# Optimization experiments

Measured on AMD Instinct MI355X. Metric: run time of the kernel, lower is better.

The kernel has to match this reference:

```python
import jax, jax.numpy as jnp
import numpy as np

N_NODES = 100000
N_EDGES = 3200000
D_FEAT = 128


def setup_inputs() -> dict:
    key = jax.random.key(0)
    k1, k2, k3, k4 = jax.random.split(key, 4)
    row = jax.random.randint(k1, (N_EDGES,), 0, N_NODES, dtype=jnp.int32)
    col = jax.random.randint(k2, (N_EDGES,), 0, N_NODES, dtype=jnp.int32)
    vals = jax.random.uniform(k3, (N_EDGES,), dtype=jnp.float32)
    embeds = jax.random.normal(k4, (N_NODES, D_FEAT), dtype=jnp.float32)
    return {"row": row, "col": col, "vals": vals, "embeds": embeds}


def reference(row, col, vals, embeds):
    # torch.spmm(adj, embeds) with adj in COO form (row, col, vals):
    # out[i, :] = sum_{e : row[e]==i} vals[e] * embeds[col[e], :]
    msgs = embeds[col] * vals[:, None]          # [E, d] gather + scale
    out = jax.ops.segment_sum(msgs, row, num_segments=embeds.shape[0])  # [N, d]
    return out
```

## Files before the change

kernel.cpp:

```cpp
#include <hip/hip_runtime.h>
#include <hip/hip_fp16.h>

#define D_FEAT 128

constexpr int SCAN_BLOCK = 256;
constexpr int SCAN_ITEMS = 8;
constexpr int SCAN_CHUNK = SCAN_BLOCK * SCAN_ITEMS;

constexpr int BUCKET_SHIFT = 7;
constexpr int TILE_ROWS = 1 << BUCKET_SHIFT;
constexpr int NB_MAX = 1024;
constexpr int PART_TILE = 4096;
constexpr int CAP = 6144;

__global__ void __launch_bounds__(256) spmm_atomic_kernel(
    const int* __restrict__ row, const int* __restrict__ col,
    const float* __restrict__ vals, const float* __restrict__ embeds,
    float* __restrict__ out, int n_edges)
{
    const int lane = threadIdx.x & 63;
    const int wave_in_block = threadIdx.x >> 6;
    const int waves_per_block = blockDim.x >> 6;
    const int n_waves = gridDim.x * waves_per_block;
    for (int e = blockIdx.x * waves_per_block + wave_in_block; e < n_edges; e += n_waves) {
        const int r = row[e];
        const int c = col[e];
        const float v = vals[e];
        const float2 emb = *reinterpret_cast<const float2*>(&embeds[(size_t)c * D_FEAT + lane * 2]);
        float* o = &out[(size_t)r * D_FEAT + lane * 2];
        atomicAdd(o, emb.x * v);
        atomicAdd(o + 1, emb.y * v);
    }
}


__global__ void __launch_bounds__(256) bucket_hist_kernel(
    const int* __restrict__ row, int* __restrict__ bucket_counts, int n_edges, int nb)
{
    __shared__ int cnt[NB_MAX];
    for (int b = threadIdx.x; b < nb; b += 256) cnt[b] = 0;
    __syncthreads();
    const int i = blockIdx.x * blockDim.x + threadIdx.x;
    const int stride = gridDim.x * blockDim.x;
    const int n4 = n_edges >> 2;
    for (int k = i; k < n4; k += stride) {
        int4 r4 = reinterpret_cast<const int4*>(row)[k];
        atomicAdd(&cnt[r4.x >> BUCKET_SHIFT], 1);
        atomicAdd(&cnt[r4.y >> BUCKET_SHIFT], 1);
        atomicAdd(&cnt[r4.z >> BUCKET_SHIFT], 1);
        atomicAdd(&cnt[r4.w >> BUCKET_SHIFT], 1);
    }
    for (int k = (n4 << 2) + i; k < n_edges; k += stride)
        atomicAdd(&cnt[row[k] >> BUCKET_SHIFT], 1);
    __syncthreads();
    for (int b = threadIdx.x; b < nb; b += 256) {
        int c = cnt[b];
        if (c) atomicAdd(&bucket_counts[b], c);
    }
}

__global__ void __launch_bounds__(1024) bucket_scan_kernel(
    const int* __restrict__ bucket_counts, int* __restrict__ bucket_ptr,
    int* __restrict__ bucket_fill, int nb)
{
    __shared__ int lds[1024];
    const int t = threadIdx.x;
    lds[t] = (t < nb) ? bucket_counts[t] : 0;
    __syncthreads();
    for (int off = 1; off < 1024; off <<= 1) {
        int x = (t >= off) ? lds[t - off] : 0;
        __syncthreads();
        lds[t] += x;
        __syncthreads();
    }
    const int excl = (t == 0) ? 0 : lds[t - 1];
    if (t <= nb) bucket_ptr[t] = excl;
    if (t < nb)  bucket_fill[t] = excl;
}

__global__ void __launch_bounds__(256) bucket_init_padded_kernel(
    int* __restrict__ bucket_ptr, int* __restrict__ bucket_fill, int nb, int cap_b)
{
    int b = blockIdx.x * blockDim.x + threadIdx.x;
    if (b < nb) {
        bucket_ptr[b]  = b * cap_b;
        bucket_fill[b] = b * cap_b;
    }
}

__global__ void __launch_bounds__(256) partition_kernel(
    const int* __restrict__ row, const int* __restrict__ col, const float* __restrict__ vals,
    int* __restrict__ bucket_fill, uint2* __restrict__ tmp, int n_edges, int nb)
{
    __shared__ int cnt[NB_MAX];
    __shared__ int start[NB_MAX];
    const int tid = threadIdx.x;
    const int base = blockIdx.x * PART_TILE;

    for (int b = tid; b < NB_MAX; b += 256) cnt[b] = 0;
    __syncthreads();

    #pragma unroll
    for (int k = 0; k < PART_TILE / 1024; ++k) {
        int idx = (base >> 2) + k * 256 + tid;
        if (idx * 4 + 3 < n_edges) {
            int4 r4 = reinterpret_cast<const int4*>(row)[idx];
            atomicAdd(&cnt[r4.x >> BUCKET_SHIFT], 1);
            atomicAdd(&cnt[r4.y >> BUCKET_SHIFT], 1);
            atomicAdd(&cnt[r4.z >> BUCKET_SHIFT], 1);
            atomicAdd(&cnt[r4.w >> BUCKET_SHIFT], 1);
        } else {
            for (int j = 0; j < 4; ++j) {
                int e = idx * 4 + j;
                if (e < n_edges) atomicAdd(&cnt[row[e] >> BUCKET_SHIFT], 1);
            }
        }
    }
    __syncthreads();

    for (int b = tid; b < nb; b += 256) {
        int c = cnt[b];
        if (c > 0) start[b] = atomicAdd(&bucket_fill[b], c);
    }
    __syncthreads();

    #pragma unroll
    for (int k = 0; k < PART_TILE / 1024; ++k) {
        int idx = (base >> 2) + k * 256 + tid;
        if (idx * 4 + 3 < n_edges) {
            int4  r4 = reinterpret_cast<const int4*>(row)[idx];
            int4  c4 = reinterpret_cast<const int4*>(col)[idx];
            float4 v4 = reinterpret_cast<const float4*>(vals)[idx];
            const int rs[4]   = {r4.x, r4.y, r4.z, r4.w};
            const int cs[4]   = {c4.x, c4.y, c4.z, c4.w};
            const float vs[4] = {v4.x, v4.y, v4.z, v4.w};
            #pragma unroll
            for (int j = 0; j < 4; ++j) {
                int r = rs[j];
                int b = r >> BUCKET_SHIFT;
                int slot = atomicSub(&cnt[b], 1) - 1;
                unsigned hb = (unsigned)__half_as_ushort(__float2half(vs[j]));
                uint2 p;
                p.x = ((unsigned)(r & (TILE_ROWS - 1)) << 17) | (unsigned)cs[j];
                p.y = hb | (hb << 16);
                tmp[start[b] + slot] = p;
            }
        } else {
            for (int j = 0; j < 4; ++j) {
                int e = idx * 4 + j;
                if (e < n_edges) {
                    int r = row[e];
                    int b = r >> BUCKET_SHIFT;
                    int slot = atomicSub(&cnt[b], 1) - 1;
                    unsigned hb = (unsigned)__half_as_ushort(__float2half(vals[e]));
                    uint2 p;
                    p.x = ((unsigned)(r & (TILE_ROWS - 1)) << 17) | (unsigned)col[e];
                    p.y = hb | (hb << 16);
                    tmp[start[b] + slot] = p;
                }
            }
        }
    }
}

__global__ void __launch_bounds__(256) convert_kernel(
    const float* __restrict__ embeds, unsigned short* __restrict__ out16, int n4)
{
    int i = blockIdx.x * blockDim.x + threadIdx.x;
    int stride = gridDim.x * blockDim.x;
    for (; i < n4; i += stride) {
        float4 f = *reinterpret_cast<const float4*>(&embeds[(size_t)i * 4]);
        ushort4 o;
        o.x = __half_as_ushort(__float2half(f.x));
        o.y = __half_as_ushort(__float2half(f.y));
        o.z = __half_as_ushort(__float2half(f.z));
        o.w = __half_as_ushort(__float2half(f.w));
        *reinterpret_cast<ushort4*>(&out16[(size_t)i * 4]) = o;
    }
}

__device__ __forceinline__ __half2 u2h2(unsigned u)
{
    return *reinterpret_cast<__half2*>(&u);
}

__global__ void __launch_bounds__(1024, 8) spmm_bucket_sorted_kernel(
    const uint2* __restrict__ tmp, const int* __restrict__ bucket_ptr,
    const int* __restrict__ bucket_fill,
    const unsigned short* __restrict__ embeds16, float* __restrict__ out, int n_nodes)
{
    __shared__ uint2 sedge[CAP];
    __shared__ int cnt[TILE_ROWS];
    __shared__ int rstart[TILE_ROWS];
    __shared__ int rcur[TILE_ROWS];
    __shared__ int sscan[TILE_ROWS];

    const int b = blockIdx.x;
    const int lo = bucket_ptr[b];
    const int hi = bucket_fill[b];
    const int t = threadIdx.x;
    const int lane = t & 63;
    const int h = lane >> 5;
    const int lq = lane & 31;
    const int w = t >> 6;

    __half2 acc[16];
    #pragma unroll
    for (int i = 0; i < 16; ++i) acc[i] = __float2half2_rn(0.f);

    for (int cur = lo; cur < hi; cur += CAP) {
        const int bcount = min(CAP, hi - cur);

        uint2 e[6];
        #pragma unroll
        for (int k = 0; k < 6; ++k) {
            int idx = t + k * 1024;
            if (idx < bcount) e[k] = tmp[cur + idx];
        }
        if (t < TILE_ROWS) { cnt[t] = 0; rcur[t] = 0; }
        __syncthreads();

        #pragma unroll
        for (int k = 0; k < 6; ++k) {
            int idx = t + k * 1024;
            if (idx < bcount) atomicAdd(&cnt[(e[k].x >> 17) & (TILE_ROWS - 1)], 1);
        }
        __syncthreads();

        if (t < TILE_ROWS) sscan[t] = cnt[t];
        __syncthreads();
        for (int off = 1; off < TILE_ROWS; off <<= 1) {
            int v = 0;
            if (t < TILE_ROWS && t >= off) v = sscan[t - off];
            __syncthreads();
            if (t < TILE_ROWS) sscan[t] += v;
            __syncthreads();
        }
        if (t < TILE_ROWS) rstart[t] = sscan[t] - cnt[t];
        __syncthreads();

        #pragma unroll
        for (int k = 0; k < 6; ++k) {
            int idx = t + k * 1024;
            if (idx < bcount) {
                int rl = (e[k].x >> 17) & (TILE_ROWS - 1);
                int pos = rstart[rl] + atomicAdd(&rcur[rl], 1);
                sedge[pos] = uint2{e[k].x & 0x1FFFFu, e[k].y};
            }
        }
        __syncthreads();

        #pragma unroll
        for (int rr = 0; rr < 8; ++rr) {
            const int r = w * 8 + rr;
            const int js = rstart[r];
            const int je = js + cnt[r];
            int j = js;
            for (; j + 7 < je; j += 8) {
                uint2 q0 = sedge[j + 0 + h];
                uint2 q1 = sedge[j + 2 + h];
                uint2 q2 = sedge[j + 4 + h];
                uint2 q3 = sedge[j + 6 + h];
                uint2 u0 = *reinterpret_cast<const uint2*>(&embeds16[((size_t)q0.x << 7) + lq * 4]);
                uint2 u1 = *reinterpret_cast<const uint2*>(&embeds16[((size_t)q1.x << 7) + lq * 4]);
                uint2 u2 = *reinterpret_cast<const uint2*>(&embeds16[((size_t)q2.x << 7) + lq * 4]);
                uint2 u3 = *reinterpret_cast<const uint2*>(&embeds16[((size_t)q3.x << 7) + lq * 4]);
                acc[2*rr]   = __hfma2(u2h2(q0.y), u2h2(u0.x), acc[2*rr]);
                acc[2*rr+1] = __hfma2(u2h2(q0.y), u2h2(u0.y), acc[2*rr+1]);
                acc[2*rr]   = __hfma2(u2h2(q1.y), u2h2(u1.x), acc[2*rr]);
                acc[2*rr+1] = __hfma2(u2h2(q1.y), u2h2(u1.y), acc[2*rr+1]);
                acc[2*rr]   = __hfma2(u2h2(q2.y), u2h2(u2.x), acc[2*rr]);
                acc[2*rr+1] = __hfma2(u2h2(q2.y), u2h2(u2.y), acc[2*rr+1]);
                acc[2*rr]   = __hfma2(u2h2(q3.y), u2h2(u3.x), acc[2*rr]);
                acc[2*rr+1] = __hfma2(u2h2(q3.y), u2h2(u3.y), acc[2*rr+1]);
            }
            for (; j + 1 < je; j += 2) {
                uint2 q = sedge[j + h];
                uint2 u = *reinterpret_cast<const uint2*>(&embeds16[((size_t)q.x << 7) + lq * 4]);
                acc[2*rr]   = __hfma2(u2h2(q.y), u2h2(u.x), acc[2*rr]);
                acc[2*rr+1] = __hfma2(u2h2(q.y), u2h2(u.y), acc[2*rr+1]);
            }
            if (j < je && h == 0) {
                uint2 q = sedge[j];
                uint2 u = *reinterpret_cast<const uint2*>(&embeds16[((size_t)q.x << 7) + lq * 4]);
                acc[2*rr]   = __hfma2(u2h2(q.y), u2h2(u.x), acc[2*rr]);
                acc[2*rr+1] = __hfma2(u2h2(q.y), u2h2(u.y), acc[2*rr+1]);
            }
        }
        __syncthreads();
    }

    float4 facc[8];
    #pragma unroll
    for (int rr = 0; rr < 8; ++rr) {
        float2 a = __half22float2(acc[2*rr]);
        float2 bq = __half22float2(acc[2*rr+1]);
        facc[rr] = float4{a.x, a.y, bq.x, bq.y};
        facc[rr].x += __shfl_xor(facc[rr].x, 32);
        facc[rr].y += __shfl_xor(facc[rr].y, 32);
        facc[rr].z += __shfl_xor(facc[rr].z, 32);
        facc[rr].w += __shfl_xor(facc[rr].w, 32);
    }

    const int rbase = b << BUCKET_SHIFT;
    #pragma unroll
    for (int k = 0; k < 4; ++k) {
        float4 a0 = facc[k];
        float4 a1 = facc[k + 4];
        float4 vv;
        vv.x = h ? a1.x : a0.x;
        vv.y = h ? a1.y : a0.y;
        vv.z = h ? a1.z : a0.z;
        vv.w = h ? a1.w : a0.w;
        int r = rbase + w * 8 + k + 4 * h;
        if (r < n_nodes)
            *reinterpret_cast<float4*>(&out[(size_t)r * D_FEAT + lq * 4]) = vv;
    }
}

__global__ void hist_kernel(const int* __restrict__ row, int* __restrict__ counts, int n)
{
    int i = blockIdx.x * blockDim.x + threadIdx.x;
    int stride = gridDim.x * blockDim.x;
    for (; i < n; i += stride) atomicAdd(&counts[row[i]], 1);
}

__global__ void __launch_bounds__(SCAN_BLOCK) scan1_kernel(
    const int* __restrict__ counts, int* __restrict__ scan_out,
    int* __restrict__ chunk_sums, int n)
{
    __shared__ int lds[SCAN_BLOCK];
    const int chunk = blockIdx.x;
    const int base = chunk * SCAN_CHUNK;
    const int tbase = base + threadIdx.x * SCAN_ITEMS;

    int pref[SCAN_ITEMS];
    int tsum = 0;
    for (int k = 0; k < SCAN_ITEMS; ++k) {
        int idx = tbase + k;
        int v = (idx < n) ? counts[idx] : 0;
        pref[k] = tsum;
        tsum += v;
    }
    lds[threadIdx.x] = tsum;
    __syncthreads();
    for (int off = 1; off < SCAN_BLOCK; off <<= 1) {
        int v = (threadIdx.x >= off) ? lds[threadIdx.x - off] : 0;
        __syncthreads();
        lds[threadIdx.x] += v;
        __syncthreads();
    }
    const int texcl = (threadIdx.x == 0) ? 0 : lds[threadIdx.x - 1];
    for (int k = 0; k < SCAN_ITEMS; ++k) {
        int idx = tbase + k;
        if (idx < n) scan_out[idx] = texcl + pref[k];
    }
    if (threadIdx.x == SCAN_BLOCK - 1) chunk_sums[chunk] = lds[SCAN_BLOCK - 1];
}

__global__ void scan2_kernel(int* chunk_sums, int nchunks)
{
    if (blockIdx.x == 0 && threadIdx.x == 0) {
        int acc = 0;
        for (int i = 0; i < nchunks; ++i) { int v = chunk_sums[i]; chunk_sums[i] = acc; acc += v; }
    }
}

__global__ void scan3_kernel(int* __restrict__ row_ptr, const int* __restrict__ chunk_sums,
                             int n, int n_edges)
{
    int i = blockIdx.x * blockDim.x + threadIdx.x;
    if (i < n) row_ptr[i] += chunk_sums[i / SCAN_CHUNK];
    if (i == 0) row_ptr[n] = n_edges;
}

__global__ void scatter_kernel(const int* __restrict__ row, const int* __restrict__ col,
                               const float* __restrict__ vals,
                               const int* __restrict__ row_ptr, int* __restrict__ row_fill,
                               uint2* __restrict__ sorted_cv, int n_edges)
{
    int i = blockIdx.x * blockDim.x + threadIdx.x;
    int stride = gridDim.x * blockDim.x;
    for (; i < n_edges; i += stride) {
        int r = row[i];
        int pos = row_ptr[r] + atomicAdd(&row_fill[r], 1);
        uint2 cv;
        cv.x = (unsigned)col[i];
        cv.y = __float_as_uint(vals[i]);
        sorted_cv[pos] = cv;
    }
}

__global__ void __launch_bounds__(256) spmm_csr_kernel(
    const int* __restrict__ row_ptr, const uint2* __restrict__ sorted_cv,
    const float* __restrict__ embeds, float* __restrict__ out, int n_rows)
{
    const int lane = threadIdx.x & 63;
    const int wid = (blockIdx.x * blockDim.x + threadIdx.x) >> 6;
    const int n_waves = (gridDim.x * blockDim.x) >> 6;

    for (int r = wid; r < n_rows; r += n_waves) {
        const int start = row_ptr[r];
        const int end   = row_ptr[r + 1];
        float2 acc = {0.f, 0.f};
        for (int j = start; j < end; ++j) {
            uint2 cv = sorted_cv[j];
            const float2 e = *reinterpret_cast<const float2*>(&embeds[(size_t)cv.x * D_FEAT + lane * 2]);
            const float v = __uint_as_float(cv.y);
            acc.x += v * e.x;
            acc.y += v * e.y;
        }
        *reinterpret_cast<float2*>(&out[(size_t)r * D_FEAT + lane * 2]) = acc;
    }
}

extern "C" void kernel_launch(void* const* d_in, const int* in_sizes, int n_in,
                              void* d_out, int out_size, void* d_ws, size_t ws_size,
                              hipStream_t stream) {
    const int*   row    = (const int*)d_in[0];
    const int*   col    = (const int*)d_in[1];
    const float* vals   = (const float*)d_in[2];
    const float* embeds = (const float*)d_in[3];
    float*       out    = (float*)d_out;

    const int n_edges = in_sizes[0];
    const int n_nodes = in_sizes[3] / D_FEAT;
    const int nchunks = (n_nodes + SCAN_CHUNK - 1) / SCAN_CHUNK;
    const int nb = (n_nodes + TILE_ROWS - 1) >> BUCKET_SHIFT;

    const int avg = n_edges / (nb > 0 ? nb : 1);
    const int cap_b = avg + avg / 4 + 256;

    char* base = (char*)d_ws;

    size_t offP = 0;
    uint2* tmpP           = (uint2*)(base + offP);             offP += ((size_t)nb * cap_b * 8 + 255) & ~(size_t)255;
    unsigned short* emb16P = (unsigned short*)(base + offP);   offP += ((size_t)n_nodes * D_FEAT * 2 + 255) & ~(size_t)255;
    int* bptrP            = (int*)(base + offP);               offP += (size_t)(nb + 1) * 4;
    int* bfillP           = (int*)(base + offP);               offP += (size_t)(nb + 1) * 4;

    size_t offS = 0;
    uint2* tmpS           = (uint2*)(base + offS);             offS += ((size_t)n_edges * 8 + 255) & ~(size_t)255;
    unsigned short* emb16S = (unsigned short*)(base + offS);   offS += ((size_t)n_nodes * D_FEAT * 2 + 255) & ~(size_t)255;
    int* bcntS            = (int*)(base + offS);               offS += (size_t)(nb + 1) * 4;
    int* bptrS            = (int*)(base + offS);               offS += (size_t)(nb + 1) * 4;
    int* bfillS           = (int*)(base + offS);               offS += (size_t)(nb + 1) * 4;

    const bool common_ok = (nb <= 1023) && (n_nodes < (1 << 17));
    const bool padded_ok  = common_ok && (offP <= ws_size);
    const bool scanned_ok = common_ok && (offS <= ws_size);

    if (!padded_ok && !scanned_ok) {
        size_t off2 = 0;
        uint2* s_cv = (uint2*)(base + off2); off2 += (size_t)n_edges * 8;
        int* rc  = (int*)(base + off2); off2 += (size_t)n_nodes * 4;
        int* rf  = (int*)(base + off2); off2 += (size_t)n_nodes * 4;
        int* rp  = (int*)(base + off2); off2 += (size_t)(n_nodes + 1) * 4;
        int* cs  = (int*)(base + off2); off2 += (size_t)nchunks * 4;
        if (off2 > ws_size) {
            hipMemsetAsync(d_out, 0, (size_t)out_size * sizeof(float), stream);
            spmm_atomic_kernel<<<2048, 256, 0, stream>>>(row, col, vals, embeds, out, n_edges);
            return;
        }
        hipMemsetAsync(rc, 0, (size_t)n_nodes * 2 * sizeof(int), stream);
        hist_kernel<<<2048, 256, 0, stream>>>(row, rc, n_edges);
        scan1_kernel<<<nchunks, SCAN_BLOCK, 0, stream>>>(rc, rp, cs, n_nodes);
        scan2_kernel<<<1, 64, 0, stream>>>(cs, nchunks);
        scan3_kernel<<<(n_nodes + 256) / 256, 256, 0, stream>>>(rp, cs, n_nodes, n_edges);
        scatter_kernel<<<2048, 256, 0, stream>>>(row, col, vals, rp, rf, s_cv, n_edges);
        spmm_csr_kernel<<<4096, 256, 0, stream>>>(rp, s_cv, embeds, out, n_nodes);
        return;
    }

    uint2* tmp;
    unsigned short* embeds16;
    int *bptr, *bfill;

    const int part_blocks = (n_edges + PART_TILE - 1) / PART_TILE;

    if (padded_ok) {
        tmp = tmpP; embeds16 = emb16P; bptr = bptrP; bfill = bfillP;
        bucket_init_padded_kernel<<<(nb + 255) / 256, 256, 0, stream>>>(bptr, bfill, nb, cap_b);
    } else {
        tmp = tmpS; embeds16 = emb16S; bptr = bptrS; bfill = bfillS;
        hipMemsetAsync(bcntS, 0, (size_t)(nb + 1) * sizeof(int), stream);
        bucket_hist_kernel<<<512, 256, 0, stream>>>(row, bcntS, n_edges, nb);
        bucket_scan_kernel<<<1, 1024, 0, stream>>>(bcntS, bptr, bfill, nb);
    }

    partition_kernel<<<part_blocks, 256, 0, stream>>>(row, col, vals, bfill, tmp, n_edges, nb);

    const int n4 = n_nodes * D_FEAT / 4;
    convert_kernel<<<4096, 256, 0, stream>>>(embeds, embeds16, n4);

    spmm_bucket_sorted_kernel<<<nb, 1024, 0, stream>>>(tmp, bptr, bfill, embeds16, out, n_nodes);
}
```

Before: 232.9 us.

## Halve bucket size and use persistent work-queue SpMM blocks with 16-lane row groups

Buckets now cover 64 rows instead of 128, which doubles the bucket count and halves the per-chunk edge capacity. The final SpMM kernel becomes persistent: 1024 blocks of 512 threads pull buckets from a global atomic counter. Each quarter-wave of 16 lanes handles a whole edge with 16-byte embedding loads, and partial sums are reduced across quarter-waves with shuffles. The aim is better load balance, wider per-lane loads, and cheaper in-block row sorting via a wave-level shuffle scan. In exchange it adds per-bucket barriers, a second pass over edges from global memory rather than registers, and extra shuffle reductions.

```diff
diff --git a/kernel.cpp b/kernel.cpp
--- a/kernel.cpp
+++ b/kernel.cpp
@@ -7,11 +7,11 @@
 constexpr int SCAN_ITEMS = 8;
 constexpr int SCAN_CHUNK = SCAN_BLOCK * SCAN_ITEMS;
 
-constexpr int BUCKET_SHIFT = 7;
+constexpr int BUCKET_SHIFT = 6;
 constexpr int TILE_ROWS = 1 << BUCKET_SHIFT;
-constexpr int NB_MAX = 1024;
+constexpr int NB_MAX = 2048;
 constexpr int PART_TILE = 4096;
-constexpr int CAP = 6144;
+constexpr int CAP = 3072;
 
 __global__ void __launch_bounds__(256) spmm_atomic_kernel(
     const int* __restrict__ row, const int* __restrict__ col,
@@ -65,7 +65,9 @@
 {
     __shared__ int lds[1024];
     const int t = threadIdx.x;
-    lds[t] = (t < nb) ? bucket_counts[t] : 0;
+    int c0 = (2 * t     < nb) ? bucket_counts[2 * t]     : 0;
+    int c1 = (2 * t + 1 < nb) ? bucket_counts[2 * t + 1] : 0;
+    lds[t] = c0 + c1;
     __syncthreads();
     for (int off = 1; off < 1024; off <<= 1) {
         int x = (t >= off) ? lds[t - off] : 0;
@@ -73,9 +75,10 @@
         lds[t] += x;
         __syncthreads();
     }
-    const int excl = (t == 0) ? 0 : lds[t - 1];
-    if (t <= nb) bucket_ptr[t] = excl;
-    if (t < nb)  bucket_fill[t] = excl;
+    const int excl = lds[t] - c0 - c1;
+    if (2 * t < nb)     { bucket_ptr[2 * t]     = excl;      bucket_fill[2 * t]     = excl; }
+    if (2 * t + 1 < nb) { bucket_ptr[2 * t + 1] = excl + c0; bucket_fill[2 * t + 1] = excl + c0; }
+    if (t == 1023) bucket_ptr[nb] = lds[1023];
 }
 
 __global__ void __launch_bounds__(256) bucket_init_padded_kernel(
@@ -97,7 +100,7 @@
     const int tid = threadIdx.x;
     const int base = blockIdx.x * PART_TILE;
 
-    for (int b = tid; b < NB_MAX; b += 256) cnt[b] = 0;
+    for (int b = tid; b < nb; b += 256) cnt[b] = 0;
     __syncthreads();
 
     #pragma unroll
@@ -184,137 +187,135 @@
     return *reinterpret_cast<__half2*>(&u);
 }
 
-__global__ void __launch_bounds__(1024, 8) spmm_bucket_sorted_kernel(
+__global__ void __launch_bounds__(512, 6) spmm_bucket_q_kernel(
     const uint2* __restrict__ tmp, const int* __restrict__ bucket_ptr,
-    const int* __restrict__ bucket_fill,
-    const unsigned short* __restrict__ embeds16, float* __restrict__ out, int n_nodes)
+    const int* __restrict__ bucket_fill, int* __restrict__ qcounter,
+    const unsigned short* __restrict__ embeds16, float* __restrict__ out,
+    int n_nodes, int nb)
 {
     __shared__ uint2 sedge[CAP];
     __shared__ int cnt[TILE_ROWS];
     __shared__ int rstart[TILE_ROWS];
     __shared__ int rcur[TILE_ROWS];
-    __shared__ int sscan[TILE_ROWS];
-
-    const int b = blockIdx.x;
-    const int lo = bucket_ptr[b];
-    const int hi = bucket_fill[b];
+    __shared__ int sbucket;
+
     const int t = threadIdx.x;
     const int lane = t & 63;
-    const int h = lane >> 5;
-    const int lq = lane & 31;
+    const int q = lane >> 4;
+    const int lq = lane & 15;
     const int w = t >> 6;
 
-    __half2 acc[16];
-    #pragma unroll
-    for (int i = 0; i < 16; ++i) acc[i] = __float2half2_rn(0.f);
-
-    for (int cur = lo; cur < hi; cur += CAP) {
-        const int bcount = min(CAP, hi - cur);
-
-        uint2 e[6];
+    for (;;) {
+        if (t == 0) sbucket = atomicAdd(qcounter, 1);
+        __syncthreads();
+        const int b = sbucket;
+        if (b >= nb) break;
+        const int lo = bucket_ptr[b];
+        const int hi = bucket_fill[b];
+
+        __half2 acc[32];
         #pragma unroll
-        for (int k = 0; k < 6; ++k) {
-            int idx = t + k * 1024;
-            if (idx < bcount) e[k] = tmp[cur + idx];
-        }
-        if (t < TILE_ROWS) { cnt[t] = 0; rcur[t] = 0; }
-        __syncthreads();
-
-        #pragma unroll
-        for (int k = 0; k < 6; ++k) {
-            int idx = t + k * 1024;
-            if (idx < bcount) atomicAdd(&cnt[(e[k].x >> 17) & (TILE_ROWS - 1)], 1);
-        }
-        __syncthreads();
-
-        if (t < TILE_ROWS) sscan[t] = cnt[t];
-        __syncthreads();
-        for (int off = 1; off < TILE_ROWS; off <<= 1) {
-            int v = 0;
-            if (t < TILE_ROWS && t >= off) v = sscan[t - off];
+        for (int i = 0; i < 32; ++i) acc[i] = __float2half2_rn(0.f);
+
+        for (int cur = lo; cur < hi; cur += CAP) {
+            const int bcount = min(CAP, hi - cur);
+
+            if (t < TILE_ROWS) cnt[t] = 0;
             __syncthreads();
-            if (t < TILE_ROWS) sscan[t] += v;
+
+            for (int idx = t; idx < bcount; idx += 512)
+                atomicAdd(&cnt[(tmp[cur + idx].x >> 17) & (TILE_ROWS - 1)], 1);
             __syncthreads();
-        }
-        if (t < TILE_ROWS) rstart[t] = sscan[t] - cnt[t];
-        __syncthreads();
-
-        #pragma unroll
-        for (int k = 0; k < 6; ++k) {
-            int idx = t + k * 1024;
-            if (idx < bcount) {
-                int rl = (e[k].x >> 17) & (TILE_ROWS - 1);
+
+            if (w == 0) {
+                int v = cnt[lane];
+                int inc = v;
+                #pragma unroll
+                for (int off = 1; off < 64; off <<= 1) {
+                    int x = __shfl_up(inc, off);
+                    if (lane >= off) inc += x;
+                }
+                rstart[lane] = inc - v;
+                rcur[lane] = 0;
+            }
+            __syncthreads();
+
+            for (int idx = t; idx < bcount; idx += 512) {
+                uint2 p = tmp[cur + idx];
+                int rl = (p.x >> 17) & (TILE_ROWS - 1);
                 int pos = rstart[rl] + atomicAdd(&rcur[rl], 1);
-                sedge[pos] = uint2{e[k].x & 0x1FFFFu, e[k].y};
+                sedge[pos] = uint2{p.x & 0x1FFFFu, p.y};
             }
-        }
-        __syncthreads();
-
+            __syncthreads();
+
+            #pragma unroll
+            for (int rr = 0; rr < 8; ++rr) {
+                const int r = w * 8 + rr;
+                const int js = rstart[r];
+                const int je = js + cnt[r];
+                int j = js + q;
+                for (; j + 4 < je; j += 8) {
+                    uint2 e0 = sedge[j];
+                    uint2 e1 = sedge[j + 4];
+                    uint4 u0 = *reinterpret_cast<const uint4*>(&embeds16[((size_t)e0.x << 7) + lq * 8]);
+                    uint4 u1 = *reinterpret_cast<const uint4*>(&embeds16[((size_t)e1.x << 7) + lq * 8]);
+                    const __half2 v0 = u2h2(e0.y);
+                    const __half2 v1 = u2h2(e1.y);
+                    acc[4*rr+0] = __hfma2(v0, u2h2(u0.x), acc[4*rr+0]);
+                    acc[4*rr+1] = __hfma2(v0, u2h2(u0.y), acc[4*rr+1]);
+                    acc[4*rr+2] = __hfma2(v0, u2h2(u0.z), acc[4*rr+2]);
+                    acc[4*rr+3] = __hfma2(v0, u2h2(u0.w), acc[4*rr+3]);
+                    acc[4*rr+0] = __hfma2(v1, u2h2(u1.x), acc[4*rr+0]);
+                    acc[4*rr+1] = __hfma2(v1, u2h2(u1.y), acc[4*rr+1]);
+                    acc[4*rr+2] = __hfma2(v1, u2h2(u1.z), acc[4*rr+2]);
+                    acc[4*rr+3] = __hfma2(v1, u2h2(u1.w), acc[4*rr+3]);
+                }
+                if (j < je) {
+                    uint2 e0 = sedge[j];
+                    uint4 u0 = *reinterpret_cast<const uint4*>(&embeds16[((size_t)e0.x << 7) + lq * 8]);
+                    const __half2 v0 = u2h2(e0.y);
+                    acc[4*rr+0] = __hfma2(v0, u2h2(u0.x), acc[4*rr+0]);
+                    acc[4*rr+1] = __hfma2(v0, u2h2(u0.y), acc[4*rr+1]);
+                    acc[4*rr+2] = __hfma2(v0, u2h2(u0.z), acc[4*rr+2]);
+                    acc[4*rr+3] = __hfma2(v0, u2h2(u0.w), acc[4*rr+3]);
+                }
+            }
+            __syncthreads();
+        }
+
+        float4 oa0, oa1, ob0, ob1;
+        oa0 = oa1 = ob0 = ob1 = float4{0.f, 0.f, 0.f, 0.f};
         #pragma unroll
         for (int rr = 0; rr < 8; ++rr) {
-            const int r = w * 8 + rr;
-            const int js = rstart[r];
-            const int je = js + cnt[r];
-            int j = js;
-            for (; j + 7 < je; j += 8) {
-                uint2 q0 = sedge[j + 0 + h];
-                uint2 q1 = sedge[j + 2 + h];
-                uint2 q2 = sedge[j + 4 + h];
-                uint2 q3 = sedge[j + 6 + h];
-                uint2 u0 = *reinterpret_cast<const uint2*>(&embeds16[((size_t)q0.x << 7) + lq * 4]);
-                uint2 u1 = *reinterpret_cast<const uint2*>(&embeds16[((size_t)q1.x << 7) + lq * 4]);
-                uint2 u2 = *reinterpret_cast<const uint2*>(&embeds16[((size_t)q2.x << 7) + lq * 4]);
-                uint2 u3 = *reinterpret_cast<const uint2*>(&embeds16[((size_t)q3.x << 7) + lq * 4]);
-                acc[2*rr]   = __hfma2(u2h2(q0.y), u2h2(u0.x), acc[2*rr]);
-                acc[2*rr+1] = __hfma2(u2h2(q0.y), u2h2(u0.y), acc[2*rr+1]);
-                acc[2*rr]   = __hfma2(u2h2(q1.y), u2h2(u1.x), acc[2*rr]);
-                acc[2*rr+1] = __hfma2(u2h2(q1.y), u2h2(u1.y), acc[2*rr+1]);
-                acc[2*rr]   = __hfma2(u2h2(q2.y), u2h2(u2.x), acc[2*rr]);
-                acc[2*rr+1] = __hfma2(u2h2(q2.y), u2h2(u2.y), acc[2*rr+1]);
-                acc[2*rr]   = __hfma2(u2h2(q3.y), u2h2(u3.x), acc[2*rr]);
-                acc[2*rr+1] = __hfma2(u2h2(q3.y), u2h2(u3.y), acc[2*rr+1]);
-            }
-            for (; j + 1 < je; j += 2) {
-                uint2 q = sedge[j + h];
-                uint2 u = *reinterpret_cast<const uint2*>(&embeds16[((size_t)q.x << 7) + lq * 4]);
-                acc[2*rr]   = __hfma2(u2h2(q.y), u2h2(u.x), acc[2*rr]);
-                acc[2*rr+1] = __hfma2(u2h2(q.y), u2h2(u.y), acc[2*rr+1]);
-            }
-            if (j < je && h == 0) {
-                uint2 q = sedge[j];
-                uint2 u = *reinterpret_cast<const uint2*>(&embeds16[((size_t)q.x << 7) + lq * 4]);
-                acc[2*rr]   = __hfma2(u2h2(q.y), u2h2(u.x), acc[2*rr]);
-                acc[2*rr+1] = __hfma2(u2h2(q.y), u2h2(u.y), acc[2*rr+1]);
-            }
+            float2 f0 = __half22float2(acc[4*rr+0]);
+            float2 f1 = __half22float2(acc[4*rr+1]);
+            float2 f2 = __half22float2(acc[4*rr+2]);
+            float2 f3 = __half22float2(acc[4*rr+3]);
+            float v0 = f0.x, v1 = f0.y, v2 = f1.x, v3 = f1.y;
+            float v4 = f2.x, v5 = f2.y, v6 = f3.x, v7 = f3.y;
+            v0 += __shfl_xor(v0, 16); v0 += __shfl_xor(v0, 32);
+            v1 += __shfl_xor(v1, 16); v1 += __shfl_xor(v1, 32);
+            v2 += __shfl_xor(v2, 16); v2 += __shfl_xor(v2, 32);
+            v3 += __shfl_xor(v3, 16); v3 += __shfl_xor(v3, 32);
+            v4 += __shfl_xor(v4, 16); v4 += __shfl_xor(v4, 32);
+            v5 += __shfl_xor(v5, 16); v5 += __shfl_xor(v5, 32);
+            v6 += __shfl_xor(v6, 16); v6 += __shfl_xor(v6, 32);
+            v7 += __shfl_xor(v7, 16); v7 += __shfl_xor(v7, 32);
+            if (rr == q)     { oa0 = float4{v0,v1,v2,v3}; oa1 = float4{v4,v5,v6,v7}; }
+            if (rr == q + 4) { ob0 = float4{v0,v1,v2,v3}; ob1 = float4{v4,v5,v6,v7}; }
+        }
+        const int rbase = b << BUCKET_SHIFT;
+        const int rA = rbase + w * 8 + q;
+        const int rB = rA + 4;
+        if (rA < n_nodes) {
+            *reinterpret_cast<float4*>(&out[(size_t)rA * D_FEAT + lq * 8])     = oa0;
+            *reinterpret_cast<float4*>(&out[(size_t)rA * D_FEAT + lq * 8 + 4]) = oa1;
+        }
+        if (rB < n_nodes) {
+            *reinterpret_cast<float4*>(&out[(size_t)rB * D_FEAT + lq * 8])     = ob0;
+            *reinterpret_cast<float4*>(&out[(size_t)rB * D_FEAT + lq * 8 + 4]) = ob1;
         }
         __syncthreads();
-    }
-
-    float4 facc[8];
-    #pragma unroll
-    for (int rr = 0; rr < 8; ++rr) {
-        float2 a = __half22float2(acc[2*rr]);
-        float2 bq = __half22float2(acc[2*rr+1]);
-        facc[rr] = float4{a.x, a.y, bq.x, bq.y};
-        facc[rr].x += __shfl_xor(facc[rr].x, 32);
-        facc[rr].y += __shfl_xor(facc[rr].y, 32);
-        facc[rr].z += __shfl_xor(facc[rr].z, 32);
-        facc[rr].w += __shfl_xor(facc[rr].w, 32);
-    }
-
-    const int rbase = b << BUCKET_SHIFT;
-    #pragma unroll
-    for (int k = 0; k < 4; ++k) {
-        float4 a0 = facc[k];
-        float4 a1 = facc[k + 4];
-        float4 vv;
-        vv.x = h ? a1.x : a0.x;
-        vv.y = h ? a1.y : a0.y;
-        vv.z = h ? a1.z : a0.z;
-        vv.w = h ? a1.w : a0.w;
-        int r = rbase + w * 8 + k + 4 * h;
-        if (r < n_nodes)
-            *reinterpret_cast<float4*>(&out[(size_t)r * D_FEAT + lq * 4]) = vv;
     }
 }
 
@@ -438,6 +439,7 @@
     unsigned short* emb16P = (unsigned short*)(base + offP);   offP += ((size_t)n_nodes * D_FEAT * 2 + 255) & ~(size_t)255;
     int* bptrP            = (int*)(base + offP);               offP += (size_t)(nb + 1) * 4;
     int* bfillP           = (int*)(base + offP);               offP += (size_t)(nb + 1) * 4;
+    int* qcntP            = (int*)(base + offP);               offP += 256;
 
     size_t offS = 0;
     uint2* tmpS           = (uint2*)(base + offS);             offS += ((size_t)n_edges * 8 + 255) & ~(size_t)255;
@@ -445,8 +447,9 @@
     int* bcntS            = (int*)(base + offS);               offS += (size_t)(nb + 1) * 4;
     int* bptrS            = (int*)(base + offS);               offS += (size_t)(nb + 1) * 4;
     int* bfillS           = (int*)(base + offS);               offS += (size_t)(nb + 1) * 4;
-
-    const bool common_ok = (nb <= 1023) && (n_nodes < (1 << 17));
+    int* qcntS            = (int*)(base + offS);               offS += 256;
+
+    const bool common_ok = (nb <= 2047) && (n_nodes < (1 << 17));
     const bool padded_ok  = common_ok && (offP <= ws_size);
     const bool scanned_ok = common_ok && (offS <= ws_size);
 
@@ -474,24 +477,26 @@
 
     uint2* tmp;
     unsigned short* embeds16;
-    int *bptr, *bfill;
+    int *bptr, *bfill, *qcnt;
 
     const int part_blocks = (n_edges + PART_TILE - 1) / PART_TILE;
 
     if (padded_ok) {
-        tmp = tmpP; embeds16 = emb16P; bptr = bptrP; bfill = bfillP;
+        tmp = tmpP; embeds16 = emb16P; bptr = bptrP; bfill = bfillP; qcnt = qcntP;
         bucket_init_padded_kernel<<<(nb + 255) / 256, 256, 0, stream>>>(bptr, bfill, nb, cap_b);
     } else {
-        tmp = tmpS; embeds16 = emb16S; bptr = bptrS; bfill = bfillS;
+        tmp = tmpS; embeds16 = emb16S; bptr = bptrS; bfill = bfillS; qcnt = qcntS;
         hipMemsetAsync(bcntS, 0, (size_t)(nb + 1) * sizeof(int), stream);
         bucket_hist_kernel<<<512, 256, 0, stream>>>(row, bcntS, n_edges, nb);
         bucket_scan_kernel<<<1, 1024, 0, stream>>>(bcntS, bptr, bfill, nb);
     }
+    hipMemsetAsync(qcnt, 0, sizeof(int), stream);
 
     partition_kernel<<<part_blocks, 256, 0, stream>>>(row, col, vals, bfill, tmp, n_edges, nb);
 
     const int n4 = n_nodes * D_FEAT / 4;
     convert_kernel<<<4096, 256, 0, stream>>>(embeds, embeds16, n4);
 
-    spmm_bucket_sorted_kernel<<<nb, 1024, 0, stream>>>(tmp, bptr, bfill, embeds16, out, n_nodes);
-}
+    spmm_bucket_q_kernel<<<1024, 512, 0, stream>>>(tmp, bptr, bfill, qcnt,
+                                                   embeds16, out, n_nodes, nb);
+}
```

After: 341.7 us. 1.47x slower.
